# Kernel optimization log

Measured on AMD Instinct MI355X. Metric: run time of the kernel, lower is better.

## Reference

```python
import jax, jax.numpy as jnp
import numpy as np

TAU = 0.07          # temperature
TOP_N_SIM = 5       # n_neighb for KNN label assignment
RANKING_K = 4       # top-k same/diff-class sims for confidence ratio


def setup_inputs() -> dict:
    key = jax.random.key(0)
    k1, k2, k3 = jax.random.split(key, 3)
    n_src, n_tgt, d, n_cls = 8192, 6144, 256, 64
    return {
        "source_features": jax.random.normal(k1, (n_src, d), dtype=jnp.float32),
        "source_labels": jax.random.randint(k2, (n_src,), 0, n_cls, dtype=jnp.int32),
        "target_features": jax.random.normal(k3, (n_tgt, d), dtype=jnp.float32),
    }


def _l2_normalize(x):
    # F.normalize(x, dim=1, p=2) with eps=1e-12
    n = jnp.sqrt(jnp.sum(x * x, axis=1, keepdims=True))
    return x / jnp.maximum(n, 1e-12)


def reference(source_features, source_labels, target_features):
    n_tgt = target_features.shape[0]
    top_ranked_n = n_tgt * 2 // 3

    # cosine similarity matrix [n_src, n_tgt]
    sim = _l2_normalize(source_features) @ _l2_normalize(target_features).T

    # sort each column descending over sources
    order = jnp.argsort(-sim, axis=0)                      # [S, T]

    # KNN label assignment with torch.mode semantics (tie -> smallest value)
    neigh = source_labels[order[:TOP_N_SIM]]               # [K, T]
    counts = (neigh[:, None, :] == neigh[None, :, :]).sum(axis=1)  # [K, T]
    maxc = counts.max(axis=0)                              # [T]
    big = jnp.iinfo(source_labels.dtype).max
    assigned = jnp.where(counts == maxc[None, :], neigh, big).min(axis=0)  # [T]

    # sims & labels reordered by descending similarity, per column
    sorted_sims = jnp.take_along_axis(sim, order, axis=0)  # [S, T]
    sorted_labels = source_labels[order]                   # [S, T]
    pos = sorted_labels == assigned[None, :]               # [S, T]

    def first_k_masked_sum(mask):
        # sum of first RANKING_K sorted sims where mask is True, per column
        csum = jnp.cumsum(mask.astype(sim.dtype), axis=0)
        sel = mask & (csum <= RANKING_K)
        return jnp.sum(jnp.where(sel, sorted_sims, 0.0), axis=0)

    nln = first_k_masked_sum(pos)
    nun = first_k_masked_sum(~pos)
    scores = jax.lax.stop_gradient(nln / nun)              # [T], detached

    _, top_ind = jax.lax.top_k(scores, top_ranked_n)       # confident targets
    conf_sim = sim[:, top_ind]                             # [S, top_ranked_n]
    conf_lab = assigned[top_ind]

    # contrastive softmax loss over sources
    mask_sim = (source_labels[:, None] == conf_lab[None, :]).astype(sim.dtype)
    exp_scores = jax.nn.softmax(conf_sim / TAU, axis=0)
    contrastive = (exp_scores * mask_sim).sum(axis=0) / exp_scores.sum(axis=0)
    return -jnp.mean(jnp.log(contrastive + 1e-6))
```

## Files before the change

### kernel.cpp

```cpp
#include <hip/hip_runtime.h>
#include <cstdint>
#include <cstddef>

#define DIM 256
#define NSRC 8192
#define NCLS 64
#define KSTEPS 8
#define INV_TAU (1.0f / 0.07f)
#define EPITCH 136

typedef __attribute__((ext_vector_type(8))) short bf16x8;
typedef __attribute__((ext_vector_type(4))) float f32x4;
typedef unsigned char uchar;

__device__ __forceinline__ ushort f2bf_rne(float f) {
    uint u = __float_as_uint(f);
    uint r = u + 0x7fff + ((u >> 16) & 1);
    return (ushort)(r >> 16);
}
__device__ __forceinline__ uint bf2ord(uint u) {
    return u ^ (0x8000u + (u >> 15) * 0x7FFFu);
}
__device__ __forceinline__ float ord2f(uint o) {
    uint u = (o & 0x8000u) ? (o ^ 0x8000u) : (~o & 0xFFFFu);
    return __uint_as_float(u << 16);
}
__device__ __forceinline__ uint med3u(uint a, uint b, uint c) {
    uint d;
    asm("v_med3_u32 %0, %1, %2, %3" : "=v"(d) : "v"(a), "v"(b), "v"(c));
    return d;
}

__device__ __forceinline__ void gload_lds16(const void* g, void* l) {
    __builtin_amdgcn_global_load_lds((const __attribute__((address_space(1))) void*)g,
                                     (__attribute__((address_space(3))) void*)l,
                                     16, 0, 0);
}

__global__ __launch_bounds__(256) void l2bf2_k(const float* __restrict__ inA,
                                               ushort* __restrict__ outA, int nA,
                                               const float* __restrict__ inB,
                                               ushort* __restrict__ outB, int nB) {
    const int w = (blockIdx.x * 256 + threadIdx.x) >> 6;
    const int lane = threadIdx.x & 63;
    if (w >= nA + nB) return;
    const float* in;
    ushort* out;
    int row;
    if (w < nA) { in = inA; out = outA; row = w; }
    else        { in = inB; out = outB; row = w - nA; }
    float4 v = *(const float4*)(in + (size_t)row * DIM + lane * 4);
    float ss = v.x * v.x + v.y * v.y + v.z * v.z + v.w * v.w;
#pragma unroll
    for (int d = 1; d < 64; d <<= 1) ss += __shfl_xor(ss, d);
    const float n = fmaxf(sqrtf(ss), 1e-12f);
    ushort4 o;
    o.x = f2bf_rne(v.x / n);
    o.y = f2bf_rne(v.y / n);
    o.z = f2bf_rne(v.z / n);
    o.w = f2bf_rne(v.w / n);
    *(ushort4*)(out + (size_t)row * DIM + lane * 4) = o;
}

__global__ __launch_bounds__(256) void class_build_k(const int* __restrict__ labels,
                                                     uchar* __restrict__ lab8,
                                                     int* __restrict__ cstart,
                                                     int* __restrict__ clist, int n) {
    const int c = blockIdx.x, t = threadIdx.x;
    const int g = c * 256 + t;
    if (g < n) lab8[g] = (uchar)labels[g];

    __shared__ int sl[256], se[256];
    const int per = n >> 8;
    const int i0 = t * per;
    int less = 0, eq = 0;
    for (int j = 0; j < per; ++j) {
        const int l = labels[i0 + j];
        less += (l < c);
        eq += (l == c);
    }
    sl[t] = less; se[t] = eq;
    __syncthreads();
    for (int s = 1; s < 256; s <<= 1) {
        const int a = (t >= s) ? sl[t - s] : 0;
        const int b = (t >= s) ? se[t - s] : 0;
        __syncthreads();
        sl[t] += a; se[t] += b;
        __syncthreads();
    }
    const int base = sl[255];
    int pos = base + se[t] - eq;
    for (int j = 0; j < per; ++j) {
        const int i = i0 + j;
        if (labels[i] == c) clist[pos++] = i;
    }
    if (t == 0) cstart[c] = base;
    if (c == 0 && t == 1) cstart[NCLS] = n;
}

__global__ __launch_bounds__(512) void gemm_mfma_k(const ushort* __restrict__ A,
                                                   const ushort* __restrict__ B,
                                                   ushort* __restrict__ C,
                                                   int M, int N) {
    __shared__ __align__(16) ushort smem[24576];

    const int tid = threadIdx.x;
    const int lane = tid & 63, wid = tid >> 6;
    const int wr = wid >> 1, wc = wid & 1;

    const int gx = gridDim.x;
    const int bid = blockIdx.y * gx + blockIdx.x;
    const int rowsPerX = gridDim.y >> 3;
    const int grpW = 8;
    const int grpSize = rowsPerX * grpW;
    const int xcd = bid & 7;
    const int local = bid >> 3;
    const int grp = local / grpSize;
    const int within = local % grpSize;
    const int bm = (xcd * rowsPerX + within % rowsPerX) * 128;
    const int bn = (grp * grpW + within / rowsPerX) * 128;

    const int cr = tid >> 2;
    const int cch = tid & 3;
    const int sch = cch ^ ((cr >> 1) & 3);
    const char* aSrcP = (const char*)A + (size_t)(bm + cr) * (DIM * 2) + sch * 16;
    const char* bSrcP = (const char*)B + (size_t)(bn + cr) * (DIM * 2) + sch * 16;
    const uint ldsOff = (uint)(wid * 1024);

    const int fr = lane & 15, fk = lane >> 4;
    const int swz = (fr >> 1) & 3;
    int idxA[2], idxB[4];
#pragma unroll
    for (int m = 0; m < 2; ++m)
        idxA[m] = (wr * 32 + m * 16 + fr) * 32 + ((fk ^ swz) * 8);
#pragma unroll
    for (int n = 0; n < 4; ++n)
        idxB[n] = (wc * 64 + n * 16 + fr) * 32 + ((fk ^ swz) * 8);

    f32x4 acc[2][4];
#pragma unroll
    for (int m = 0; m < 2; ++m)
#pragma unroll
        for (int n = 0; n < 4; ++n) acc[m][n] = (f32x4){0.f, 0.f, 0.f, 0.f};

#define STAGE(b, ks)                                                               \
    {                                                                              \
        gload_lds16(aSrcP + (ks) * 64, (char*)smem + (b) * 8192 + ldsOff);         \
        gload_lds16(bSrcP + (ks) * 64, (char*)smem + 24576 + (b) * 8192 + ldsOff); \
    }

    STAGE(0, 0);
    STAGE(1, 1);

#pragma unroll
    for (int ks = 0; ks < KSTEPS; ++ks) {
        if (ks < KSTEPS - 1) { asm volatile("s_waitcnt vmcnt(2)" ::: "memory"); }
        else                 { asm volatile("s_waitcnt vmcnt(0)" ::: "memory"); }
        __builtin_amdgcn_s_barrier();
        asm volatile("" ::: "memory");

        if (ks + 2 < KSTEPS) STAGE((ks + 2) % 3, ks + 2);

        const int slot = ks % 3;
        const ushort* sAc = smem + slot * 4096;
        const ushort* sBc = smem + 12288 + slot * 4096;
        bf16x8 av[2], bv[4];
#pragma unroll
        for (int m = 0; m < 2; ++m) av[m] = *(const bf16x8*)&sAc[idxA[m]];
#pragma unroll
        for (int n = 0; n < 4; ++n) bv[n] = *(const bf16x8*)&sBc[idxB[n]];
#pragma unroll
        for (int m = 0; m < 2; ++m)
#pragma unroll
            for (int n = 0; n < 4; ++n)
                acc[m][n] = __builtin_amdgcn_mfma_f32_16x16x32_bf16(av[m], bv[n], acc[m][n], 0, 0, 0);
    }
#undef STAGE

    __syncthreads();
#pragma unroll
    for (int m = 0; m < 2; ++m) {
#pragma unroll
        for (int n = 0; n < 4; ++n) {
            const int colb = wc * 64 + n * 16 + fr;
#pragma unroll
            for (int j = 0; j < 4; ++j) {
                const int rowb = wr * 32 + m * 16 + fk * 4 + j;
                smem[rowb * EPITCH + colb] = f2bf_rne(acc[m][n][j]);
            }
        }
    }
    __syncthreads();
    const int rr = tid >> 4, cc = (tid & 15) * 8;
#pragma unroll
    for (int it = 0; it < 4; ++it) {
        const int r = it * 32 + rr;
        uint4 v = *(const uint4*)&smem[r * EPITCH + cc];
        *(uint4*)(C + (size_t)(bm + r) * N + bn + cc) = v;
    }
}

__global__ __launch_bounds__(256) void assign_score_w(const ushort* __restrict__ sim,
                                                      const int* __restrict__ labels,
                                                      const uchar* __restrict__ lab8,
                                                      const int* __restrict__ cstart,
                                                      const int* __restrict__ clist,
                                                      float* __restrict__ scores_out,
                                                      float* __restrict__ logt_out) {
    const int lane = threadIdx.x & 63, wid = threadIdx.x >> 6;
    const int t = blockIdx.x * 4 + wid;
    const ushort* row = sim + (size_t)t * NSRC;

    uint kA0 = 0, kA1 = 0, kA2 = 0, kA3 = 0;
    uint kB0 = 0, kB1 = 0, kB2 = 0, kB3 = 0;
    float s1a = 0.f, s1b = 0.f;

#define CH4X(u16, idx, K0, K1, K2, K3, S1)                              \
    {                                                                   \
        uint uu = (uint)(u16);                                          \
        float vv = __uint_as_float(uu << 16);                           \
        S1 += __expf(fmaf(vv, INV_TAU, -INV_TAU));                      \
        uint od = uu ^ (0x8000u + (uu >> 15) * 0x7FFFu);                \
        uint nk = (od << 16) | (uint)(8191 - (idx));                    \
        uint q1 = med3u(nk, K0, K1);                                    \
        uint q2 = med3u(nk, K1, K2);                                    \
        uint q3 = med3u(nk, K2, K3);                                    \
        K0 = max(K0, nk); K1 = q1; K2 = q2; K3 = q3;                    \
    }
#define CH8(u16, idx)                                                   \
    {                                                                   \
        uint uu = (uint)(u16);                                          \
        uint od = uu ^ (0x8000u + (uu >> 15) * 0x7FFFu);                \
        uint nk = (od << 16) | (uint)(8191 - (idx));                    \
        uint q1 = med3u(nk, k0, k1);                                    \
        uint q2 = med3u(nk, k1, k2);                                    \
        uint q3 = med3u(nk, k2, k3);                                    \
        uint q4 = med3u(nk, k3, k4);                                    \
        uint q5 = med3u(nk, k4, k5);                                    \
        uint q6 = med3u(nk, k5, k6);                                    \
        uint q7 = med3u(nk, k6, k7);                                    \
        k0 = max(k0, nk);                                               \
        k1 = q1; k2 = q2; k3 = q3; k4 = q4; k5 = q5; k6 = q6; k7 = q7;  \
    }
#define MERGE8                                                                     \
    _Pragma("unroll")                                                              \
    for (int d = 1; d < 64; d <<= 1) {                                             \
        uint b0 = __shfl_xor(k0, d), b1 = __shfl_xor(k1, d), b2 = __shfl_xor(k2, d),\
             b3 = __shfl_xor(k3, d), b4 = __shfl_xor(k4, d), b5 = __shfl_xor(k5, d),\
             b6 = __shfl_xor(k6, d), b7 = __shfl_xor(k7, d);                        \
        uint r0 = max(k0, b0);                                                     \
        uint r1 = max(max(min(k0, b0), k1), b1);                                   \
        uint r2 = max(max(min(k0, b1), min(k1, b0)), max(k2, b2));                 \
        uint r3 = max(max(min(k0, b2), min(k1, b1)),                               \
                      max(max(min(k2, b0), k3), b3));                              \
        uint r4 = max(max(max(min(k0, b3), min(k1, b2)),                           \
                          max(min(k2, b1), min(k3, b0))), max(k4, b4));            \
        uint r5 = max(max(max(min(k0, b4), min(k1, b3)),                           \
                          max(min(k2, b2), min(k3, b1))),                          \
                      max(max(min(k4, b0), k5), b5));                              \
        uint r6 = max(max(max(min(k0, b5), min(k1, b4)),                           \
                          max(min(k2, b3), min(k3, b2))),                          \
                      max(max(min(k4, b1), min(k5, b0)), max(k6, b6)));            \
        uint r7 = max(max(max(min(k0, b6), min(k1, b5)),                           \
                          max(min(k2, b4), min(k3, b3))),                          \
                      max(max(min(k4, b2), min(k5, b1)),                           \
                          max(max(min(k6, b0), k7), b7)));                         \
        k0 = r0; k1 = r1; k2 = r2; k3 = r3; k4 = r4; k5 = r5; k6 = r6; k7 = r7;    \
    }

    for (int i0 = lane * 8; i0 < NSRC; i0 += 1024) {
        uint4 w = *(const uint4*)(row + i0);
        uint4 w2 = *(const uint4*)(row + i0 + 512);
        CH4X(w.x & 0xFFFF, i0 + 0, kA0, kA1, kA2, kA3, s1a);
        CH4X(w.x >> 16,    i0 + 1, kA0, kA1, kA2, kA3, s1a);
        CH4X(w.y & 0xFFFF, i0 + 2, kA0, kA1, kA2, kA3, s1a);
        CH4X(w.y >> 16,    i0 + 3, kA0, kA1, kA2, kA3, s1a);
        CH4X(w.z & 0xFFFF, i0 + 4, kA0, kA1, kA2, kA3, s1a);
        CH4X(w.z >> 16,    i0 + 5, kA0, kA1, kA2, kA3, s1a);
        CH4X(w.w & 0xFFFF, i0 + 6, kA0, kA1, kA2, kA3, s1a);
        CH4X(w.w >> 16,    i0 + 7, kA0, kA1, kA2, kA3, s1a);
        CH4X(w2.x & 0xFFFF, i0 + 512, kB0, kB1, kB2, kB3, s1b);
        CH4X(w2.x >> 16,    i0 + 513, kB0, kB1, kB2, kB3, s1b);
        CH4X(w2.y & 0xFFFF, i0 + 514, kB0, kB1, kB2, kB3, s1b);
        CH4X(w2.y >> 16,    i0 + 515, kB0, kB1, kB2, kB3, s1b);
        CH4X(w2.z & 0xFFFF, i0 + 516, kB0, kB1, kB2, kB3, s1b);
        CH4X(w2.z >> 16,    i0 + 517, kB0, kB1, kB2, kB3, s1b);
        CH4X(w2.w & 0xFFFF, i0 + 518, kB0, kB1, kB2, kB3, s1b);
        CH4X(w2.w >> 16,    i0 + 519, kB0, kB1, kB2, kB3, s1b);
    }
    uint k0 = max(kA0, kB0);
    uint k1 = max(max(min(kA0, kB0), kA1), kB1);
    uint k2 = max(max(min(kA0, kB1), min(kA1, kB0)), max(kA2, kB2));
    uint k3 = max(max(min(kA0, kB2), min(kA1, kB1)),
                  max(max(min(kA2, kB0), kA3), kB3));
    uint k4 = 0, k5 = 0, k6 = 0, k7 = 0;

    const uint prek3 = k3;
    MERGE8;
    if (!__all((int)(prek3 <= k7))) {
        k0 = k1 = k2 = k3 = k4 = k5 = k6 = k7 = 0;
        for (int i0 = lane * 8; i0 < NSRC; i0 += 512) {
            uint4 w = *(const uint4*)(row + i0);
            CH8(w.x & 0xFFFF, i0 + 0); CH8(w.x >> 16, i0 + 1);
            CH8(w.y & 0xFFFF, i0 + 2); CH8(w.y >> 16, i0 + 3);
            CH8(w.z & 0xFFFF, i0 + 4); CH8(w.z >> 16, i0 + 5);
            CH8(w.w & 0xFFFF, i0 + 6); CH8(w.w >> 16, i0 + 7);
        }
        MERGE8;
    }
#undef CH4X
#undef CH8
#undef MERGE8

    float s1 = s1a + s1b;
#pragma unroll
    for (int d = 1; d < 64; d <<= 1) s1 += __shfl_xor(s1, d);

    const int l0 = labels[8191 - (int)(k0 & 0xFFFF)];
    const int l1 = labels[8191 - (int)(k1 & 0xFFFF)];
    const int l2 = labels[8191 - (int)(k2 & 0xFFFF)];
    const int l3 = labels[8191 - (int)(k3 & 0xFFFF)];
    const int l4 = labels[8191 - (int)(k4 & 0xFFFF)];
    const int l5 = labels[8191 - (int)(k5 & 0xFFFF)];
    const int l6 = labels[8191 - (int)(k6 & 0xFFFF)];
    const int l7 = labels[8191 - (int)(k7 & 0xFFFF)];

    const int c0 = 1 + (l0 == l1) + (l0 == l2) + (l0 == l3) + (l0 == l4);
    const int c1 = (l1 == l0) + 1 + (l1 == l2) + (l1 == l3) + (l1 == l4);
    const int c2 = (l2 == l0) + (l2 == l1) + 1 + (l2 == l3) + (l2 == l4);
    const int c3 = (l3 == l0) + (l3 == l1) + (l3 == l2) + 1 + (l3 == l4);
    const int c4 = (l4 == l0) + (l4 == l1) + (l4 == l2) + (l4 == l3) + 1;
    const int maxc = max(max(max(c0, c1), max(c2, c3)), c4);
    int assigned = 0x7fffffff;
    if (c0 == maxc) assigned = min(assigned, l0);
    if (c1 == maxc) assigned = min(assigned, l1);
    if (c2 == maxc) assigned = min(assigned, l2);
    if (c3 == maxc) assigned = min(assigned, l3);
    if (c4 == maxc) assigned = min(assigned, l4);
    const int aL = assigned;

    const int negcnt = (l0 != aL) + (l1 != aL) + (l2 != aL) + (l3 != aL) +
                       (l4 != aL) + (l5 != aL) + (l6 != aL) + (l7 != aL);
    float nun = 0.f;
    if (negcnt >= 4) {
        int c = 0;
#define NSTEP(kj, lj)                                                       \
        {                                                                   \
            bool take = ((lj) != aL) && (c < 4);                            \
            nun += take ? ord2f((kj) >> 16) : 0.f;                          \
            c += take ? 1 : 0;                                              \
        }
        NSTEP(k0, l0) NSTEP(k1, l1) NSTEP(k2, l2) NSTEP(k3, l3)
        NSTEP(k4, l4) NSTEP(k5, l5) NSTEP(k6, l6) NSTEP(k7, l7)
#undef NSTEP
    } else {
        uint n0 = 0, n1 = 0, n2 = 0, n3 = 0;
        for (int i0 = lane * 8; i0 < NSRC; i0 += 512) {
            uint4 w = *(const uint4*)(row + i0);
            uint2 lw = *(const uint2*)(lab8 + i0);
#define NEGP(u16, lb)                                                       \
            {                                                               \
                uint uu = (uint)(u16);                                      \
                uint od = uu ^ (0x8000u + (uu >> 15) * 0x7FFFu);            \
                uint x = ((lb) == aL) ? 0u : od;                            \
                uint q1 = med3u(x, n0, n1);                                 \
                uint q2 = med3u(x, n1, n2);                                 \
                uint q3 = med3u(x, n2, n3);                                 \
                n0 = max(n0, x); n1 = q1; n2 = q2; n3 = q3;                 \
            }
            NEGP(w.x & 0xFFFF, (int)(lw.x & 255));
            NEGP(w.x >> 16,    (int)((lw.x >> 8) & 255));
            NEGP(w.y & 0xFFFF, (int)((lw.x >> 16) & 255));
            NEGP(w.y >> 16,    (int)(lw.x >> 24));
            NEGP(w.z & 0xFFFF, (int)(lw.y & 255));
            NEGP(w.z >> 16,    (int)((lw.y >> 8) & 255));
            NEGP(w.w & 0xFFFF, (int)((lw.y >> 16) & 255));
            NEGP(w.w >> 16,    (int)(lw.y >> 24));
#undef NEGP
        }
#pragma unroll
        for (int d = 1; d < 64; d <<= 1) {
            uint b0 = __shfl_xor(n0, d), b1 = __shfl_xor(n1, d),
                 b2 = __shfl_xor(n2, d), b3 = __shfl_xor(n3, d);
            uint r0 = max(n0, b0);
            uint r1 = max(max(min(n0, b0), n1), b1);
            uint r2 = max(max(min(n0, b1), min(n1, b0)), max(n2, b2));
            uint r3 = max(max(min(n0, b2), min(n1, b1)),
                          max(max(min(n2, b0), n3), b3));
            n0 = r0; n1 = r1; n2 = r2; n3 = r3;
        }
        nun = (n0 ? ord2f(n0) : 0.f) + (n1 ? ord2f(n1) : 0.f) +
              (n2 ? ord2f(n2) : 0.f) + (n3 ? ord2f(n3) : 0.f);
    }

    const int cs = cstart[aL], ce = cstart[aL + 1];
    float tp0 = -2.f, tp1 = -2.f, tp2 = -2.f, tp3 = -2.f;
    float sp = 0.f;
    for (int p = cs + lane; p < ce; p += 64) {
        const int idx = clist[p];
        float v = __uint_as_float(((uint)row[idx]) << 16);
        sp += __expf(fmaf(v, INV_TAU, -INV_TAU));
        float q1 = __builtin_amdgcn_fmed3f(v, tp0, tp1);
        float q2 = __builtin_amdgcn_fmed3f(v, tp1, tp2);
        float q3 = __builtin_amdgcn_fmed3f(v, tp2, tp3);
        tp0 = fmaxf(tp0, v); tp1 = q1; tp2 = q2; tp3 = q3;
    }
#pragma unroll
    for (int d = 1; d < 64; d <<= 1) {
        sp += __shfl_xor(sp, d);
        float b0 = __shfl_xor(tp0, d), b1 = __shfl_xor(tp1, d),
              b2 = __shfl_xor(tp2, d), b3 = __shfl_xor(tp3, d);
        float r0 = fmaxf(tp0, b0);
        float r1 = fmaxf(fmaxf(fminf(tp0, b0), tp1), b1);
        float r2 = fmaxf(fmaxf(fminf(tp0, b1), fminf(tp1, b0)), fmaxf(tp2, b2));
        float r3 = fmaxf(fmaxf(fminf(tp0, b2), fminf(tp1, b1)),
                         fmaxf(fmaxf(fminf(tp2, b0), tp3), b3));
        tp0 = r0; tp1 = r1; tp2 = r2; tp3 = r3;
    }

    if (lane == 0) {
        float nln = (tp0 > -1.5f ? tp0 : 0.f) + (tp1 > -1.5f ? tp1 : 0.f) +
                    (tp2 > -1.5f ? tp2 : 0.f) + (tp3 > -1.5f ? tp3 : 0.f);
        scores_out[t] = nln / nun;
        logt_out[t] = logf(sp / s1 + 1e-6f);
    }
}

__global__ __launch_bounds__(256) void select_topk_w(const float* __restrict__ scores,
                                                     int* __restrict__ selected,
                                                     int n, int k) {
    const int lane = threadIdx.x & 63, wid = threadIdx.x >> 6;
    const int t = blockIdx.x * 4 + wid;
    if (t >= n) return;
    const float st = scores[t];
    int rank = 0;
    for (int j0 = lane * 4; j0 < n; j0 += 256) {
        float4 v = *(const float4*)(scores + j0);
        rank += (v.x > st) || (v.x == st && (j0 + 0) < t);
        rank += (v.y > st) || (v.y == st && (j0 + 1) < t);
        rank += (v.z > st) || (v.z == st && (j0 + 2) < t);
        rank += (v.w > st) || (v.w == st && (j0 + 3) < t);
    }
    for (int d = 1; d < 64; d <<= 1) rank += __shfl_xor(rank, d);
    if (lane == 0) selected[t] = (rank < k) ? 1 : 0;
}

__global__ __launch_bounds__(256) void finalize_k(const float* __restrict__ logt,
                                                  const int* __restrict__ selected,
                                                  float* __restrict__ out, int n, int k) {
    __shared__ float red[256];
    const int tid = threadIdx.x;
    float s = 0.f;
    for (int i = tid; i < n; i += 256) s += selected[i] ? logt[i] : 0.f;
    red[tid] = s;
    __syncthreads();
    for (int st = 128; st > 0; st >>= 1) {
        if (tid < st) red[tid] += red[tid + st];
        __syncthreads();
    }
    if (tid == 0) out[0] = -red[0] / (float)k;
}

extern "C" void kernel_launch(void* const* d_in, const int* in_sizes, int n_in,
                              void* d_out, int out_size, void* d_ws, size_t ws_size,
                              hipStream_t stream) {
    const float* srcF = (const float*)d_in[0];
    const int* labels = (const int*)d_in[1];
    const float* tgtF = (const float*)d_in[2];
    float* out = (float*)d_out;

    const int n_src = in_sizes[1];
    const int d = in_sizes[0] / n_src;
    const int n_tgt = in_sizes[2] / d;
    const int topn = n_tgt * 2 / 3;

    char* ws = (char*)d_ws;
    ushort* src2 = (ushort*)ws;  ws += (size_t)n_src * DIM * sizeof(ushort);
    ushort* tgt2 = (ushort*)ws;  ws += (size_t)n_tgt * DIM * sizeof(ushort);
    ushort* sim  = (ushort*)ws;  ws += (size_t)n_tgt * NSRC * sizeof(ushort);
    float* scores = (float*)ws;  ws += (size_t)n_tgt * sizeof(float);
    float* logt   = (float*)ws;  ws += (size_t)n_tgt * sizeof(float);
    int* selected = (int*)ws;    ws += (size_t)n_tgt * sizeof(int);
    int* cstart   = (int*)ws;    ws += (size_t)(NCLS + 1) * sizeof(int);
    int* clist    = (int*)ws;    ws += (size_t)n_src * sizeof(int);
    uchar* lab8   = (uchar*)ws;  ws += (size_t)n_src;

    const int nrows = n_tgt + n_src;
    l2bf2_k<<<(nrows + 3) / 4, 256, 0, stream>>>(tgtF, tgt2, n_tgt, srcF, src2, n_src);
    class_build_k<<<NCLS, 256, 0, stream>>>(labels, lab8, cstart, clist, n_src);

    dim3 grid(n_src / 128, n_tgt / 128);
    gemm_mfma_k<<<grid, 512, 0, stream>>>(tgt2, src2, sim, n_tgt, n_src);

    assign_score_w<<<n_tgt / 4, 256, 0, stream>>>(sim, labels, lab8, cstart, clist,
                                                  scores, logt);
    select_topk_w<<<(n_tgt + 3) / 4, 256, 0, stream>>>(scores, selected, n_tgt, topn);
    finalize_k<<<1, 256, 0, stream>>>(logt, selected, out, n_tgt, topn);
}
```

Before: 110.2 us.

## Fuse per-tile top-8 selection and exp-sum into GEMM epilogue

The GEMM epilogue now scans each 128-column tile of the bf16 similarity block already staged in LDS. For every target row it builds a per-tile top-8 key list and a partial softmax exp-sum, then writes them to a partials buffer. assign_score_w no longer streams the full 8192-wide sim row for top-k. It merges the 64 partial lists by shuffle and sums the partial exp-sums. This trades a second full pass over the similarity matrix for extra epilogue work in the GEMM and a small extra partials buffer in global memory.

```diff
diff --git a/kernel.cpp b/kernel.cpp
--- a/kernel.cpp
+++ b/kernel.cpp
@@ -37,214 +37,8 @@
                                      16, 0, 0);
 }
 
-__global__ __launch_bounds__(256) void l2bf2_k(const float* __restrict__ inA,
-                                               ushort* __restrict__ outA, int nA,
-                                               const float* __restrict__ inB,
-                                               ushort* __restrict__ outB, int nB) {
-    const int w = (blockIdx.x * 256 + threadIdx.x) >> 6;
-    const int lane = threadIdx.x & 63;
-    if (w >= nA + nB) return;
-    const float* in;
-    ushort* out;
-    int row;
-    if (w < nA) { in = inA; out = outA; row = w; }
-    else        { in = inB; out = outB; row = w - nA; }
-    float4 v = *(const float4*)(in + (size_t)row * DIM + lane * 4);
-    float ss = v.x * v.x + v.y * v.y + v.z * v.z + v.w * v.w;
-#pragma unroll
-    for (int d = 1; d < 64; d <<= 1) ss += __shfl_xor(ss, d);
-    const float n = fmaxf(sqrtf(ss), 1e-12f);
-    ushort4 o;
-    o.x = f2bf_rne(v.x / n);
-    o.y = f2bf_rne(v.y / n);
-    o.z = f2bf_rne(v.z / n);
-    o.w = f2bf_rne(v.w / n);
-    *(ushort4*)(out + (size_t)row * DIM + lane * 4) = o;
-}
-
-__global__ __launch_bounds__(256) void class_build_k(const int* __restrict__ labels,
-                                                     uchar* __restrict__ lab8,
-                                                     int* __restrict__ cstart,
-                                                     int* __restrict__ clist, int n) {
-    const int c = blockIdx.x, t = threadIdx.x;
-    const int g = c * 256 + t;
-    if (g < n) lab8[g] = (uchar)labels[g];
-
-    __shared__ int sl[256], se[256];
-    const int per = n >> 8;
-    const int i0 = t * per;
-    int less = 0, eq = 0;
-    for (int j = 0; j < per; ++j) {
-        const int l = labels[i0 + j];
-        less += (l < c);
-        eq += (l == c);
-    }
-    sl[t] = less; se[t] = eq;
-    __syncthreads();
-    for (int s = 1; s < 256; s <<= 1) {
-        const int a = (t >= s) ? sl[t - s] : 0;
-        const int b = (t >= s) ? se[t - s] : 0;
-        __syncthreads();
-        sl[t] += a; se[t] += b;
-        __syncthreads();
-    }
-    const int base = sl[255];
-    int pos = base + se[t] - eq;
-    for (int j = 0; j < per; ++j) {
-        const int i = i0 + j;
-        if (labels[i] == c) clist[pos++] = i;
-    }
-    if (t == 0) cstart[c] = base;
-    if (c == 0 && t == 1) cstart[NCLS] = n;
-}
-
-__global__ __launch_bounds__(512) void gemm_mfma_k(const ushort* __restrict__ A,
-                                                   const ushort* __restrict__ B,
-                                                   ushort* __restrict__ C,
-                                                   int M, int N) {
-    __shared__ __align__(16) ushort smem[24576];
-
-    const int tid = threadIdx.x;
-    const int lane = tid & 63, wid = tid >> 6;
-    const int wr = wid >> 1, wc = wid & 1;
-
-    const int gx = gridDim.x;
-    const int bid = blockIdx.y * gx + blockIdx.x;
-    const int rowsPerX = gridDim.y >> 3;
-    const int grpW = 8;
-    const int grpSize = rowsPerX * grpW;
-    const int xcd = bid & 7;
-    const int local = bid >> 3;
-    const int grp = local / grpSize;
-    const int within = local % grpSize;
-    const int bm = (xcd * rowsPerX + within % rowsPerX) * 128;
-    const int bn = (grp * grpW + within / rowsPerX) * 128;
-
-    const int cr = tid >> 2;
-    const int cch = tid & 3;
-    const int sch = cch ^ ((cr >> 1) & 3);
-    const char* aSrcP = (const char*)A + (size_t)(bm + cr) * (DIM * 2) + sch * 16;
-    const char* bSrcP = (const char*)B + (size_t)(bn + cr) * (DIM * 2) + sch * 16;
-    const uint ldsOff = (uint)(wid * 1024);
-
-    const int fr = lane & 15, fk = lane >> 4;
-    const int swz = (fr >> 1) & 3;
-    int idxA[2], idxB[4];
-#pragma unroll
-    for (int m = 0; m < 2; ++m)
-        idxA[m] = (wr * 32 + m * 16 + fr) * 32 + ((fk ^ swz) * 8);
-#pragma unroll
-    for (int n = 0; n < 4; ++n)
-        idxB[n] = (wc * 64 + n * 16 + fr) * 32 + ((fk ^ swz) * 8);
-
-    f32x4 acc[2][4];
-#pragma unroll
-    for (int m = 0; m < 2; ++m)
-#pragma unroll
-        for (int n = 0; n < 4; ++n) acc[m][n] = (f32x4){0.f, 0.f, 0.f, 0.f};
-
-#define STAGE(b, ks)                                                               \
+#define MERGESTEP(d)                                                               \
     {                                                                              \
-        gload_lds16(aSrcP + (ks) * 64, (char*)smem + (b) * 8192 + ldsOff);         \
-        gload_lds16(bSrcP + (ks) * 64, (char*)smem + 24576 + (b) * 8192 + ldsOff); \
-    }
-
-    STAGE(0, 0);
-    STAGE(1, 1);
-
-#pragma unroll
-    for (int ks = 0; ks < KSTEPS; ++ks) {
-        if (ks < KSTEPS - 1) { asm volatile("s_waitcnt vmcnt(2)" ::: "memory"); }
-        else                 { asm volatile("s_waitcnt vmcnt(0)" ::: "memory"); }
-        __builtin_amdgcn_s_barrier();
-        asm volatile("" ::: "memory");
-
-        if (ks + 2 < KSTEPS) STAGE((ks + 2) % 3, ks + 2);
-
-        const int slot = ks % 3;
-        const ushort* sAc = smem + slot * 4096;
-        const ushort* sBc = smem + 12288 + slot * 4096;
-        bf16x8 av[2], bv[4];
-#pragma unroll
-        for (int m = 0; m < 2; ++m) av[m] = *(const bf16x8*)&sAc[idxA[m]];
-#pragma unroll
-        for (int n = 0; n < 4; ++n) bv[n] = *(const bf16x8*)&sBc[idxB[n]];
-#pragma unroll
-        for (int m = 0; m < 2; ++m)
-#pragma unroll
-            for (int n = 0; n < 4; ++n)
-                acc[m][n] = __builtin_amdgcn_mfma_f32_16x16x32_bf16(av[m], bv[n], acc[m][n], 0, 0, 0);
-    }
-#undef STAGE
-
-    __syncthreads();
-#pragma unroll
-    for (int m = 0; m < 2; ++m) {
-#pragma unroll
-        for (int n = 0; n < 4; ++n) {
-            const int colb = wc * 64 + n * 16 + fr;
-#pragma unroll
-            for (int j = 0; j < 4; ++j) {
-                const int rowb = wr * 32 + m * 16 + fk * 4 + j;
-                smem[rowb * EPITCH + colb] = f2bf_rne(acc[m][n][j]);
-            }
-        }
-    }
-    __syncthreads();
-    const int rr = tid >> 4, cc = (tid & 15) * 8;
-#pragma unroll
-    for (int it = 0; it < 4; ++it) {
-        const int r = it * 32 + rr;
-        uint4 v = *(const uint4*)&smem[r * EPITCH + cc];
-        *(uint4*)(C + (size_t)(bm + r) * N + bn + cc) = v;
-    }
-}
-
-__global__ __launch_bounds__(256) void assign_score_w(const ushort* __restrict__ sim,
-                                                      const int* __restrict__ labels,
-                                                      const uchar* __restrict__ lab8,
-                                                      const int* __restrict__ cstart,
-                                                      const int* __restrict__ clist,
-                                                      float* __restrict__ scores_out,
-                                                      float* __restrict__ logt_out) {
-    const int lane = threadIdx.x & 63, wid = threadIdx.x >> 6;
-    const int t = blockIdx.x * 4 + wid;
-    const ushort* row = sim + (size_t)t * NSRC;
-
-    uint kA0 = 0, kA1 = 0, kA2 = 0, kA3 = 0;
-    uint kB0 = 0, kB1 = 0, kB2 = 0, kB3 = 0;
-    float s1a = 0.f, s1b = 0.f;
-
-#define CH4X(u16, idx, K0, K1, K2, K3, S1)                              \
-    {                                                                   \
-        uint uu = (uint)(u16);                                          \
-        float vv = __uint_as_float(uu << 16);                           \
-        S1 += __expf(fmaf(vv, INV_TAU, -INV_TAU));                      \
-        uint od = uu ^ (0x8000u + (uu >> 15) * 0x7FFFu);                \
-        uint nk = (od << 16) | (uint)(8191 - (idx));                    \
-        uint q1 = med3u(nk, K0, K1);                                    \
-        uint q2 = med3u(nk, K1, K2);                                    \
-        uint q3 = med3u(nk, K2, K3);                                    \
-        K0 = max(K0, nk); K1 = q1; K2 = q2; K3 = q3;                    \
-    }
-#define CH8(u16, idx)                                                   \
-    {                                                                   \
-        uint uu = (uint)(u16);                                          \
-        uint od = uu ^ (0x8000u + (uu >> 15) * 0x7FFFu);                \
-        uint nk = (od << 16) | (uint)(8191 - (idx));                    \
-        uint q1 = med3u(nk, k0, k1);                                    \
-        uint q2 = med3u(nk, k1, k2);                                    \
-        uint q3 = med3u(nk, k2, k3);                                    \
-        uint q4 = med3u(nk, k3, k4);                                    \
-        uint q5 = med3u(nk, k4, k5);                                    \
-        uint q6 = med3u(nk, k5, k6);                                    \
-        uint q7 = med3u(nk, k6, k7);                                    \
-        k0 = max(k0, nk);                                               \
-        k1 = q1; k2 = q2; k3 = q3; k4 = q4; k5 = q5; k6 = q6; k7 = q7;  \
-    }
-#define MERGE8                                                                     \
-    _Pragma("unroll")                                                              \
-    for (int d = 1; d < 64; d <<= 1) {                                             \
         uint b0 = __shfl_xor(k0, d), b1 = __shfl_xor(k1, d), b2 = __shfl_xor(k2, d),\
              b3 = __shfl_xor(k3, d), b4 = __shfl_xor(k4, d), b5 = __shfl_xor(k5, d),\
              b6 = __shfl_xor(k6, d), b7 = __shfl_xor(k7, d);                        \
@@ -268,51 +62,234 @@
         k0 = r0; k1 = r1; k2 = r2; k3 = r3; k4 = r4; k5 = r5; k6 = r6; k7 = r7;    \
     }
 
-    for (int i0 = lane * 8; i0 < NSRC; i0 += 1024) {
-        uint4 w = *(const uint4*)(row + i0);
-        uint4 w2 = *(const uint4*)(row + i0 + 512);
-        CH4X(w.x & 0xFFFF, i0 + 0, kA0, kA1, kA2, kA3, s1a);
-        CH4X(w.x >> 16,    i0 + 1, kA0, kA1, kA2, kA3, s1a);
-        CH4X(w.y & 0xFFFF, i0 + 2, kA0, kA1, kA2, kA3, s1a);
-        CH4X(w.y >> 16,    i0 + 3, kA0, kA1, kA2, kA3, s1a);
-        CH4X(w.z & 0xFFFF, i0 + 4, kA0, kA1, kA2, kA3, s1a);
-        CH4X(w.z >> 16,    i0 + 5, kA0, kA1, kA2, kA3, s1a);
-        CH4X(w.w & 0xFFFF, i0 + 6, kA0, kA1, kA2, kA3, s1a);
-        CH4X(w.w >> 16,    i0 + 7, kA0, kA1, kA2, kA3, s1a);
-        CH4X(w2.x & 0xFFFF, i0 + 512, kB0, kB1, kB2, kB3, s1b);
-        CH4X(w2.x >> 16,    i0 + 513, kB0, kB1, kB2, kB3, s1b);
-        CH4X(w2.y & 0xFFFF, i0 + 514, kB0, kB1, kB2, kB3, s1b);
-        CH4X(w2.y >> 16,    i0 + 515, kB0, kB1, kB2, kB3, s1b);
-        CH4X(w2.z & 0xFFFF, i0 + 516, kB0, kB1, kB2, kB3, s1b);
-        CH4X(w2.z >> 16,    i0 + 517, kB0, kB1, kB2, kB3, s1b);
-        CH4X(w2.w & 0xFFFF, i0 + 518, kB0, kB1, kB2, kB3, s1b);
-        CH4X(w2.w >> 16,    i0 + 519, kB0, kB1, kB2, kB3, s1b);
-    }
-    uint k0 = max(kA0, kB0);
-    uint k1 = max(max(min(kA0, kB0), kA1), kB1);
-    uint k2 = max(max(min(kA0, kB1), min(kA1, kB0)), max(kA2, kB2));
-    uint k3 = max(max(min(kA0, kB2), min(kA1, kB1)),
-                  max(max(min(kA2, kB0), kA3), kB3));
-    uint k4 = 0, k5 = 0, k6 = 0, k7 = 0;
-
-    const uint prek3 = k3;
-    MERGE8;
-    if (!__all((int)(prek3 <= k7))) {
-        k0 = k1 = k2 = k3 = k4 = k5 = k6 = k7 = 0;
-        for (int i0 = lane * 8; i0 < NSRC; i0 += 512) {
-            uint4 w = *(const uint4*)(row + i0);
-            CH8(w.x & 0xFFFF, i0 + 0); CH8(w.x >> 16, i0 + 1);
-            CH8(w.y & 0xFFFF, i0 + 2); CH8(w.y >> 16, i0 + 3);
-            CH8(w.z & 0xFFFF, i0 + 4); CH8(w.z >> 16, i0 + 5);
-            CH8(w.w & 0xFFFF, i0 + 6); CH8(w.w >> 16, i0 + 7);
-        }
-        MERGE8;
-    }
-#undef CH4X
-#undef CH8
-#undef MERGE8
-
-    float s1 = s1a + s1b;
+__global__ __launch_bounds__(256) void l2bf2_k(const float* __restrict__ inA,
+                                               ushort* __restrict__ outA, int nA,
+                                               const float* __restrict__ inB,
+                                               ushort* __restrict__ outB, int nB) {
+    const int w = (blockIdx.x * 256 + threadIdx.x) >> 6;
+    const int lane = threadIdx.x & 63;
+    if (w >= nA + nB) return;
+    const float* in;
+    ushort* out;
+    int row;
+    if (w < nA) { in = inA; out = outA; row = w; }
+    else        { in = inB; out = outB; row = w - nA; }
+    float4 v = *(const float4*)(in + (size_t)row * DIM + lane * 4);
+    float ss = v.x * v.x + v.y * v.y + v.z * v.z + v.w * v.w;
+#pragma unroll
+    for (int d = 1; d < 64; d <<= 1) ss += __shfl_xor(ss, d);
+    const float n = fmaxf(sqrtf(ss), 1e-12f);
+    ushort4 o;
+    o.x = f2bf_rne(v.x / n);
+    o.y = f2bf_rne(v.y / n);
+    o.z = f2bf_rne(v.z / n);
+    o.w = f2bf_rne(v.w / n);
+    *(ushort4*)(out + (size_t)row * DIM + lane * 4) = o;
+}
+
+__global__ __launch_bounds__(256) void class_build_k(const int* __restrict__ labels,
+                                                     uchar* __restrict__ lab8,
+                                                     int* __restrict__ cstart,
+                                                     int* __restrict__ clist, int n) {
+    const int c = blockIdx.x, t = threadIdx.x;
+    const int g = c * 256 + t;
+    if (g < n) lab8[g] = (uchar)labels[g];
+
+    __shared__ int sl[256], se[256];
+    const int per = n >> 8;
+    const int i0 = t * per;
+    int less = 0, eq = 0;
+    for (int j = 0; j < per; ++j) {
+        const int l = labels[i0 + j];
+        less += (l < c);
+        eq += (l == c);
+    }
+    sl[t] = less; se[t] = eq;
+    __syncthreads();
+    for (int s = 1; s < 256; s <<= 1) {
+        const int a = (t >= s) ? sl[t - s] : 0;
+        const int b = (t >= s) ? se[t - s] : 0;
+        __syncthreads();
+        sl[t] += a; se[t] += b;
+        __syncthreads();
+    }
+    const int base = sl[255];
+    int pos = base + se[t] - eq;
+    for (int j = 0; j < per; ++j) {
+        const int i = i0 + j;
+        if (labels[i] == c) clist[pos++] = i;
+    }
+    if (t == 0) cstart[c] = base;
+    if (c == 0 && t == 1) cstart[NCLS] = n;
+}
+
+__global__ __launch_bounds__(512) void gemm_mfma_k(const ushort* __restrict__ A,
+                                                   const ushort* __restrict__ B,
+                                                   ushort* __restrict__ C,
+                                                   uint* __restrict__ part_keys,
+                                                   float* __restrict__ part_s1,
+                                                   int M, int N) {
+    __shared__ __align__(16) ushort smem[24576];
+
+    const int tid = threadIdx.x;
+    const int lane = tid & 63, wid = tid >> 6;
+    const int wr = wid >> 1, wc = wid & 1;
+
+    const int gx = gridDim.x;
+    const int bid = blockIdx.y * gx + blockIdx.x;
+    const int rowsPerX = gridDim.y >> 3;
+    const int grpW = 8;
+    const int grpSize = rowsPerX * grpW;
+    const int xcd = bid & 7;
+    const int local = bid >> 3;
+    const int grp = local / grpSize;
+    const int within = local % grpSize;
+    const int bm = (xcd * rowsPerX + within % rowsPerX) * 128;
+    const int bn = (grp * grpW + within / rowsPerX) * 128;
+
+    const int cr = tid >> 2;
+    const int cch = tid & 3;
+    const int sch = cch ^ ((cr >> 1) & 3);
+    const char* aSrcP = (const char*)A + (size_t)(bm + cr) * (DIM * 2) + sch * 16;
+    const char* bSrcP = (const char*)B + (size_t)(bn + cr) * (DIM * 2) + sch * 16;
+    const uint ldsOff = (uint)(wid * 1024);
+
+    const int fr = lane & 15, fk = lane >> 4;
+    const int swz = (fr >> 1) & 3;
+    int idxA[2], idxB[4];
+#pragma unroll
+    for (int m = 0; m < 2; ++m)
+        idxA[m] = (wr * 32 + m * 16 + fr) * 32 + ((fk ^ swz) * 8);
+#pragma unroll
+    for (int n = 0; n < 4; ++n)
+        idxB[n] = (wc * 64 + n * 16 + fr) * 32 + ((fk ^ swz) * 8);
+
+    f32x4 acc[2][4];
+#pragma unroll
+    for (int m = 0; m < 2; ++m)
+#pragma unroll
+        for (int n = 0; n < 4; ++n) acc[m][n] = (f32x4){0.f, 0.f, 0.f, 0.f};
+
+#define STAGE(b, ks)                                                               \
+    {                                                                              \
+        gload_lds16(aSrcP + (ks) * 64, (char*)smem + (b) * 8192 + ldsOff);         \
+        gload_lds16(bSrcP + (ks) * 64, (char*)smem + 24576 + (b) * 8192 + ldsOff); \
+    }
+
+    STAGE(0, 0);
+    STAGE(1, 1);
+
+#pragma unroll
+    for (int ks = 0; ks < KSTEPS; ++ks) {
+        if (ks < KSTEPS - 1) { asm volatile("s_waitcnt vmcnt(2)" ::: "memory"); }
+        else                 { asm volatile("s_waitcnt vmcnt(0)" ::: "memory"); }
+        __builtin_amdgcn_s_barrier();
+        asm volatile("" ::: "memory");
+
+        if (ks + 2 < KSTEPS) STAGE((ks + 2) % 3, ks + 2);
+
+        const int slot = ks % 3;
+        const ushort* sAc = smem + slot * 4096;
+        const ushort* sBc = smem + 12288 + slot * 4096;
+        bf16x8 av[2], bv[4];
+#pragma unroll
+        for (int m = 0; m < 2; ++m) av[m] = *(const bf16x8*)&sAc[idxA[m]];
+#pragma unroll
+        for (int n = 0; n < 4; ++n) bv[n] = *(const bf16x8*)&sBc[idxB[n]];
+#pragma unroll
+        for (int m = 0; m < 2; ++m)
+#pragma unroll
+            for (int n = 0; n < 4; ++n)
+                acc[m][n] = __builtin_amdgcn_mfma_f32_16x16x32_bf16(av[m], bv[n], acc[m][n], 0, 0, 0);
+    }
+#undef STAGE
+
+    __syncthreads();
+#pragma unroll
+    for (int m = 0; m < 2; ++m) {
+#pragma unroll
+        for (int n = 0; n < 4; ++n) {
+            const int colb = wc * 64 + n * 16 + fr;
+#pragma unroll
+            for (int j = 0; j < 4; ++j) {
+                const int rowb = wr * 32 + m * 16 + fk * 4 + j;
+                smem[rowb * EPITCH + colb] = f2bf_rne(acc[m][n][j]);
+            }
+        }
+    }
+    __syncthreads();
+    {
+        const int rr = tid >> 4, cc = (tid & 15) * 8;
+#pragma unroll
+        for (int it = 0; it < 4; ++it) {
+            const int r = it * 32 + rr;
+            uint4 v = *(const uint4*)&smem[r * EPITCH + cc];
+            *(uint4*)(C + (size_t)(bm + r) * N + bn + cc) = v;
+        }
+    }
+
+    {
+        const int rowL = wid * 16 + (lane >> 2);
+        const int colb0 = (lane & 3) * 32;
+        const int bnblk = bn >> 7;
+        const uint basekey = (uint)(8191 - bn - colb0);
+        uint k0 = 0, k1 = 0, k2 = 0, k3 = 0, k4 = 0, k5 = 0, k6 = 0, k7 = 0;
+        float s1 = 0.f;
+        const ushort* rp = &smem[rowL * EPITCH + colb0];
+#pragma unroll
+        for (int j = 0; j < 16; ++j) {
+            const uint v = *(const uint*)(rp + 2 * j);
+#pragma unroll
+            for (int h = 0; h < 2; ++h) {
+                const uint uu = (h == 0) ? (v & 0xFFFFu) : (v >> 16);
+                s1 += __expf(fmaf(__uint_as_float(uu << 16), INV_TAU, -INV_TAU));
+                const uint od = uu ^ (0x8000u + (uu >> 15) * 0x7FFFu);
+                const uint nk = (od << 16) | (basekey - (uint)(2 * j + h));
+                uint q1 = med3u(nk, k0, k1), q2 = med3u(nk, k1, k2),
+                     q3 = med3u(nk, k2, k3), q4 = med3u(nk, k3, k4),
+                     q5 = med3u(nk, k4, k5), q6 = med3u(nk, k5, k6),
+                     q7 = med3u(nk, k6, k7);
+                k0 = max(k0, nk);
+                k1 = q1; k2 = q2; k3 = q3; k4 = q4; k5 = q5; k6 = q6; k7 = q7;
+            }
+        }
+        s1 += __shfl_xor(s1, 1);
+        s1 += __shfl_xor(s1, 2);
+        MERGESTEP(1)
+        MERGESTEP(2)
+        if ((lane & 3) == 0) {
+            const size_t pb = (size_t)(bm + rowL) * 64 + bnblk;
+            uint4 lo; lo.x = k0; lo.y = k1; lo.z = k2; lo.w = k3;
+            uint4 hi; hi.x = k4; hi.y = k5; hi.z = k6; hi.w = k7;
+            *(uint4*)(part_keys + pb * 8) = lo;
+            *(uint4*)(part_keys + pb * 8 + 4) = hi;
+            part_s1[pb] = s1;
+        }
+    }
+}
+
+__global__ __launch_bounds__(256) void assign_score_w(const ushort* __restrict__ sim,
+                                                      const uint* __restrict__ part_keys,
+                                                      const float* __restrict__ part_s1,
+                                                      const int* __restrict__ labels,
+                                                      const uchar* __restrict__ lab8,
+                                                      const int* __restrict__ cstart,
+                                                      const int* __restrict__ clist,
+                                                      float* __restrict__ scores_out,
+                                                      float* __restrict__ logt_out) {
+    const int lane = threadIdx.x & 63, wid = threadIdx.x >> 6;
+    const int t = blockIdx.x * 4 + wid;
+    const ushort* row = sim + (size_t)t * NSRC;
+
+    const uint* pk = part_keys + ((size_t)t * 64 + lane) * 8;
+    uint4 lo = *(const uint4*)pk;
+    uint4 hi = *(const uint4*)(pk + 4);
+    uint k0 = lo.x, k1 = lo.y, k2 = lo.z, k3 = lo.w;
+    uint k4 = hi.x, k5 = hi.y, k6 = hi.z, k7 = hi.w;
+#pragma unroll
+    for (int d = 1; d < 64; d <<= 1) MERGESTEP(d)
+
+    float s1 = part_s1[(size_t)t * 64 + lane];
 #pragma unroll
     for (int d = 1; d < 64; d <<= 1) s1 += __shfl_xor(s1, d);
 
@@ -484,16 +461,20 @@
     int* cstart   = (int*)ws;    ws += (size_t)(NCLS + 1) * sizeof(int);
     int* clist    = (int*)ws;    ws += (size_t)n_src * sizeof(int);
     uchar* lab8   = (uchar*)ws;  ws += (size_t)n_src;
+    ws = (char*)(((uintptr_t)ws + 255) & ~(uintptr_t)255);
+    uint* part_keys = (uint*)ws; ws += (size_t)n_tgt * 64 * 8 * sizeof(uint);
+    float* part_s1  = (float*)ws; ws += (size_t)n_tgt * 64 * sizeof(float);
 
     const int nrows = n_tgt + n_src;
     l2bf2_k<<<(nrows + 3) / 4, 256, 0, stream>>>(tgtF, tgt2, n_tgt, srcF, src2, n_src);
     class_build_k<<<NCLS, 256, 0, stream>>>(labels, lab8, cstart, clist, n_src);
 
     dim3 grid(n_src / 128, n_tgt / 128);
-    gemm_mfma_k<<<grid, 512, 0, stream>>>(tgt2, src2, sim, n_tgt, n_src);
-
-    assign_score_w<<<n_tgt / 4, 256, 0, stream>>>(sim, labels, lab8, cstart, clist,
-                                                  scores, logt);
+    gemm_mfma_k<<<grid, 512, 0, stream>>>(tgt2, src2, sim, part_keys, part_s1,
+                                          n_tgt, n_src);
+
+    assign_score_w<<<n_tgt / 4, 256, 0, stream>>>(sim, part_keys, part_s1, labels,
+                                                  lab8, cstart, clist, scores, logt);
     select_topk_w<<<(n_tgt + 3) / 4, 256, 0, stream>>>(scores, selected, n_tgt, topn);
     finalize_k<<<1, 256, 0, stream>>>(logt, selected, out, n_tgt, topn);
 }
```

Result: slower. 115.1 us (+4.4%).
